# Performance work log

Hardware: AMD Instinct MI355X
Metric: run time of the kernel (lower is better)

The kernel has to match this reference:

```python
import jax, jax.numpy as jnp
import numpy as np

B = 256      # graph pairs
NPG = 28     # nodes per graph
MAXN = 32    # max_node_set_size
EPG = 64     # edges per graph (== max_edge_set_size, so no edge padding)
MAXE = 64
D = 128      # node_state_dim
FN = 32      # raw node feature dim
FE = 32      # raw edge feature dim
SK = 64      # sinkhorn_feature_dim
STEPS = 3    # propagation_steps
TEMP = 0.1
ITERS = 20
CW = 0.9     # consistency_weight
G = 2 * B
N = G * NPG
E = G * EPG


def _lin(key, fi, fo):
    return jax.random.normal(key, (fi, fo), jnp.float32) / np.sqrt(fi)


def setup_inputs() -> dict:
    key = jax.random.key(0)
    ks = jax.random.split(key, 12)
    rng = np.random.default_rng(0)
    off = (np.arange(G) * NPG)[:, None]   # graphs ordered q0,c0,q1,c1,...
    from_idx = jnp.asarray((rng.integers(0, NPG, (G, EPG)) + off).reshape(-1), jnp.int32)
    to_idx = jnp.asarray((rng.integers(0, NPG, (G, EPG)) + off).reshape(-1), jnp.int32)
    return dict(
        node_features=jax.random.normal(ks[0], (N, FN), jnp.float32),
        edge_features=jax.random.normal(ks[1], (E, FE), jnp.float32),
        enc_nw=_lin(ks[2], FN, D), enc_nb=jnp.zeros((D,), jnp.float32),
        enc_ew=_lin(ks[3], FE, D), enc_eb=jnp.zeros((D,), jnp.float32),
        msg_w1=_lin(ks[4], 3 * D, 2 * D), msg_b1=jnp.zeros((2 * D,), jnp.float32),
        msg_w2=_lin(ks[5], 2 * D, D), msg_b2=jnp.zeros((D,), jnp.float32),
        rmsg_w1=_lin(ks[6], 3 * D, 2 * D), rmsg_b1=jnp.zeros((2 * D,), jnp.float32),
        rmsg_w2=_lin(ks[7], 2 * D, D), rmsg_b2=jnp.zeros((D,), jnp.float32),
        upd_w1=_lin(ks[8], 2 * D, 2 * D), upd_b1=jnp.zeros((2 * D,), jnp.float32),
        upd_w2=_lin(ks[9], 2 * D, D), upd_b2=jnp.zeros((D,), jnp.float32),
        sk_w1=_lin(ks[10], D, SK), sk_b1=jnp.zeros((SK,), jnp.float32),
        sk_w2=_lin(ks[11], SK, SK), sk_b2=jnp.zeros((SK,), jnp.float32),
        from_idx=from_idx, to_idx=to_idx,
        query_sizes=jnp.full((B,), NPG, jnp.int32),
        corpus_sizes=jnp.full((B,), NPG, jnp.int32),
    )


def _mlp2(x, w1, b1, w2, b2):
    return jnp.maximum(x @ w1 + b1, 0.0) @ w2 + b2


def _sinkhorn(log_alpha):
    # log-domain sinkhorn (noise_factor = 0 -> deterministic)
    la = log_alpha / TEMP
    for _ in range(ITERS):
        la = la - jax.nn.logsumexp(la, axis=2, keepdims=True)
        la = la - jax.nn.logsumexp(la, axis=1, keepdims=True)
    return jnp.exp(la)


def _align(q, c, plan):
    # feature_alignment_score: -relu(q - P @ c).sum over set and feature dims
    return -jnp.maximum(q - plan @ c, 0.0).sum(axis=(1, 2))


def _forward(node_features, edge_features, enc_nw, enc_nb, enc_ew, enc_eb,
             msg_w1, msg_b1, msg_w2, msg_b2, rmsg_w1, rmsg_b1, rmsg_w2, rmsg_b2,
             upd_w1, upd_b1, upd_w2, upd_b2, sk_w1, sk_b1, sk_w2, sk_b2,
             from_idx, to_idx, query_sizes, corpus_sizes):
    h = node_features @ enc_nw + enc_nb        # encoder, [N, D]
    e = edge_features @ enc_ew + enc_eb        # [E, D]

    def messages(h):
        f = _mlp2(jnp.concatenate([h[from_idx], h[to_idx], e], -1), msg_w1, msg_b1, msg_w2, msg_b2)
        r = _mlp2(jnp.concatenate([h[to_idx], h[from_idx], e], -1), rmsg_w1, rmsg_b1, rmsg_w2, rmsg_b2)
        return f, r

    for _ in range(STEPS):  # GraphPropLayer x propagation_steps
        f, r = messages(h)
        agg = jax.ops.segment_sum(f, to_idx, num_segments=N) + \
              jax.ops.segment_sum(r, from_idx, num_segments=N)
        h = h + _mlp2(jnp.concatenate([agg, h], -1), upd_w1, upd_b1, upd_w2, upd_b2)

    # split_and_stack nodes: graphs alternate query/corpus, pad NPG -> MAXN
    hs = jnp.pad(h.reshape(B, 2, NPG, D), ((0, 0), (0, 0), (0, MAXN - NPG), (0, 0)))
    q_nodes, c_nodes = hs[:, 0], hs[:, 1]      # [B, MAXN, D]

    tq = _mlp2(q_nodes, sk_w1, sk_b1, sk_w2, sk_b2)
    tc = _mlp2(c_nodes, sk_w1, sk_b1, sk_w2, sk_b2)
    pos = jnp.arange(MAXN)[None, :]
    mq = tq * (pos < query_sizes[:, None])[..., None]
    mc = tc * (pos < corpus_sizes[:, None])[..., None]
    node_plan = _sinkhorn(jnp.einsum('bqd,bcd->bqc', mq, mc))   # [B, MAXN, MAXN]

    # propagation_messages on final node states
    f, r = messages(h)
    em = (f + r).reshape(B, 2, EPG, D)         # EPG == MAXE -> no pad
    q_edges, c_edges = em[:, 0], em[:, 1]

    # local (within-graph) endpoint indices for kronecker lookup
    fl = (from_idx % NPG).reshape(B, 2, EPG)
    tl = (to_idx % NPG).reshape(B, 2, EPG)
    qf, cf = fl[:, 0], fl[:, 1]
    qt, ct = tl[:, 0], tl[:, 1]

    def kron(T, qf, qt, cf, ct):
        straight = T[qf][:, cf] * T[qt][:, ct]   # [MAXE, MAXE]
        cross = T[qf][:, ct] * T[qt][:, cf]
        return straight + cross

    edge_scores = jax.vmap(kron)(node_plan, qf, qt, cf, ct)     # [B, MAXE, MAXE]
    edge_plan = _sinkhorn(edge_scores)

    return _align(q_nodes, c_nodes, node_plan) + CW * _align(q_edges, c_edges, edge_plan)


def reference(node_features, edge_features, enc_nw, enc_nb, enc_ew, enc_eb,
              msg_w1, msg_b1, msg_w2, msg_b2, rmsg_w1, rmsg_b1, rmsg_w2, rmsg_b2,
              upd_w1, upd_b1, upd_w2, upd_b2, sk_w1, sk_b1, sk_w2, sk_b2,
              from_idx, to_idx, query_sizes, corpus_sizes):
    return _forward(node_features, edge_features, enc_nw, enc_nb, enc_ew, enc_eb,
                    msg_w1, msg_b1, msg_w2, msg_b2, rmsg_w1, rmsg_b1, rmsg_w2, rmsg_b2,
                    upd_w1, upd_b1, upd_w2, upd_b2, sk_w1, sk_b1, sk_w2, sk_b2,
                    from_idx, to_idx, query_sizes, corpus_sizes)
```

## Files before the change

### kernel.cpp

```cpp
#include <hip/hip_runtime.h>
#include <math.h>

#define NPG 28
#define EPG 64
#define NB  256
#define NG  512
#define NN  14336
#define NE  32768
#define TEMPINV 10.0f
#define SINK_ITERS 20
#define CW 0.9f

typedef unsigned int uint;
typedef unsigned short ushort;
typedef __attribute__((ext_vector_type(8))) __bf16 bf16x8;
typedef __attribute__((ext_vector_type(4))) float f32x4;

__device__ __forceinline__ ushort f2bf(float x) {
    uint u = __float_as_uint(x);
    u += 0x7fffu + ((u >> 16) & 1u);
    return (ushort)(u >> 16);
}
__device__ __forceinline__ uint f2bf2(float lo, float hi) {
    return (uint)f2bf(lo) | ((uint)f2bf(hi) << 16);
}
__device__ __forceinline__ float bflo(uint w) { return __uint_as_float(w << 16); }
__device__ __forceinline__ float bfhi(uint w) { return __uint_as_float(w & 0xffff0000u); }
__device__ __forceinline__ uint relu_sum_pk(uint w1, uint w2, uint w3) {
    float lo = fmaxf(bflo(w1) + bflo(w2) + bflo(w3), 0.f);
    float hi = fmaxf(bfhi(w1) + bfhi(w2) + bfhi(w3), 0.f);
    return f2bf2(lo, hi);
}
__device__ __forceinline__ uint4 pack_f32x8(const float* src) {
    const float4 f0 = *(const float4*)src;
    const float4 f1 = *(const float4*)(src + 4);
    uint4 o;
    o.x = f2bf2(f0.x, f0.y);
    o.y = f2bf2(f0.z, f0.w);
    o.z = f2bf2(f1.x, f1.y);
    o.w = f2bf2(f1.z, f1.w);
    return o;
}
__device__ __forceinline__ f32x4 mfma16(bf16x8 a, bf16x8 b, f32x4 c) {
    return __builtin_amdgcn_mfma_f32_16x16x32_bf16(a, b, c, 0, 0, 0);
}

__global__ __launch_bounds__(512) void gnn_fused(
    const float* __restrict__ nf, const float* __restrict__ ef,
    const ushort* __restrict__ encL, const float* __restrict__ enc_nb,
    const ushort* __restrict__ WcombL, const float* __restrict__ bcomb,
    const ushort* __restrict__ WhpL,
    const ushort* __restrict__ W2fL, const ushort* __restrict__ W2rL,
    const float* __restrict__ b2f, const float* __restrict__ b2r,
    const ushort* __restrict__ UW1T, const float* __restrict__ ub1,
    const ushort* __restrict__ UW2T, const float* __restrict__ ub2,
    const int* __restrict__ from_idx, const int* __restrict__ to_idx,
    float* __restrict__ h, float* __restrict__ EM)
{
    __shared__ ushort HPs[NPG * 520];
    __shared__ ushort ECs[2 * 8 * 2048];
    __shared__ float acc_s[NPG * 132];
    __shared__ float hs[NPG * 132];
    __shared__ int fl[64], tl[64];
    const int g = blockIdx.x;
    const int tid = threadIdx.x;
    const int w = tid >> 6, lane = tid & 63;
    const int li = lane & 15, quad = lane >> 4;
    const int wm = w >> 1, wn = w & 1;
    ushort* hid = &HPs[0];

    if (tid < 64) {
        fl[tid] = from_idx[g * 64 + tid] - g * NPG;
        tl[tid] = to_idx[g * 64 + tid] - g * NPG;
    }

    {
        uint4 anf[2];
#pragma unroll
        for (int mi = 0; mi < 2; ++mi) {
            const int row = mi * 16 + li;
            const int rr = (row < NPG) ? row : 0;
            const float4 f0 = *(const float4*)(nf + ((size_t)g * NPG + rr) * 32 + quad * 8);
            const float4 f1 = *(const float4*)(nf + ((size_t)g * NPG + rr) * 32 + quad * 8 + 4);
            uint4 o;
            o.x = f2bf2(f0.x, f0.y); o.y = f2bf2(f0.z, f0.w);
            o.z = f2bf2(f1.x, f1.y); o.w = f2bf2(f1.z, f1.w);
            anf[mi] = o;
        }
        const int col = w * 16 + li;
        const bf16x8 b = __builtin_bit_cast(bf16x8,
            *(const uint4*)(encL + (size_t)col * 32 + quad * 8));
        f32x4 c0 = mfma16(__builtin_bit_cast(bf16x8, anf[0]), b, f32x4{0.f, 0.f, 0.f, 0.f});
        f32x4 c1 = mfma16(__builtin_bit_cast(bf16x8, anf[1]), b, f32x4{0.f, 0.f, 0.f, 0.f});
        const float bv = enc_nb[col];
#pragma unroll
        for (int r = 0; r < 4; ++r) {
            const int r0 = quad * 4 + r;
            hs[r0 * 132 + col] = c0[r] + bv;
            const int r1 = 16 + quad * 4 + r;
            if (r1 < NPG) hs[r1 * 132 + col] = c1[r] + bv;
        }
    }
    {
        uint4 aef[4];
#pragma unroll
        for (int mi = 0; mi < 4; ++mi) {
            const int e = mi * 16 + li;
            const float4 f0 = *(const float4*)(ef + ((size_t)g * 64 + e) * 32 + quad * 8);
            const float4 f1 = *(const float4*)(ef + ((size_t)g * 64 + e) * 32 + quad * 8 + 4);
            uint4 o;
            o.x = f2bf2(f0.x, f0.y); o.y = f2bf2(f0.z, f0.w);
            o.z = f2bf2(f1.x, f1.y); o.w = f2bf2(f1.z, f1.w);
            aef[mi] = o;
        }
#pragma unroll
        for (int ni = 0; ni < 4; ++ni) {
            const int col = w * 64 + ni * 16 + li;
            const bf16x8 b = __builtin_bit_cast(bf16x8,
                *(const uint4*)(WcombL + (size_t)col * 32 + quad * 8));
            const float bv = bcomb[col];
            const int pp = col >> 8, kbl = (col >> 5) & 7, j = col & 31;
#pragma unroll
            for (int mi = 0; mi < 4; ++mi) {
                f32x4 c = mfma16(__builtin_bit_cast(bf16x8, aef[mi]), b,
                                 f32x4{0.f, 0.f, 0.f, 0.f});
#pragma unroll
                for (int r = 0; r < 4; ++r) {
                    const int e = mi * 16 + quad * 4 + r;
                    ECs[pp * 16384 + kbl * 2048 + e * 32 + j] = f2bf(c[r] + bv);
                }
            }
        }
    }
    __syncthreads();

#pragma unroll 1
    for (int step = 0; step < 3; ++step) {
        uint4 ha[2][4];
#pragma unroll
        for (int mi = 0; mi < 2; ++mi) {
            const int row = mi * 16 + li;
            const int rr = (row < NPG) ? row : 0;
#pragma unroll
            for (int kb = 0; kb < 4; ++kb)
                ha[mi][kb] = pack_f32x8(&hs[rr * 132 + kb * 32 + quad * 8]);
        }
        for (int u = tid; u < NPG * 132; u += 512) acc_s[u] = 0.f;

        f32x4 acc[4];
#pragma unroll
        for (int j = 0; j < 4; ++j) acc[j] = f32x4{0.f, 0.f, 0.f, 0.f};

#pragma unroll 1
        for (int p = 0; p < 2; ++p) {
            {
                const int colw = w * 64;
#pragma unroll
                for (int ni = 0; ni < 4; ++ni) {
                    const int col = colw + ni * 16 + li;
                    const ushort* pb = WhpL + (size_t)(p * 512 + col) * 32 + quad * 8;
                    f32x4 c0 = f32x4{0.f, 0.f, 0.f, 0.f};
                    f32x4 c1 = f32x4{0.f, 0.f, 0.f, 0.f};
#pragma unroll
                    for (int kb = 0; kb < 4; ++kb) {
                        const bf16x8 b = __builtin_bit_cast(bf16x8,
                            *(const uint4*)(pb + (size_t)kb * 32768));
                        c0 = mfma16(__builtin_bit_cast(bf16x8, ha[0][kb]), b, c0);
                        c1 = mfma16(__builtin_bit_cast(bf16x8, ha[1][kb]), b, c1);
                    }
#pragma unroll
                    for (int r = 0; r < 4; ++r) {
                        const int r0 = quad * 4 + r;
                        HPs[r0 * 520 + col] = f2bf(c0[r]);
                        const int r1 = 16 + quad * 4 + r;
                        if (r1 < NPG) HPs[r1 * 520 + col] = f2bf(c1[r]);
                    }
                }
            }
            __syncthreads();

            if (p == 1) {
#pragma unroll
                for (int j = 0; j < 4; ++j) acc[j] = f32x4{0.f, 0.f, 0.f, 0.f};
            }
            const int e = wm * 16 + li;
            const int i1 = p ? tl[e] : fl[e];
            const int i2 = p ? fl[e] : tl[e];
            const int ad1 = i1 * 520 + quad * 8;
            const int ad2 = i2 * 520 + 256 + quad * 8;
            const int ade = p * 16384 + e * 32 + quad * 8;
            const ushort* W2L = p ? W2rL : W2fL;
            const int n0 = wn * 64;
            const ushort* pb[4];
#pragma unroll
            for (int ni = 0; ni < 4; ++ni)
                pb[ni] = W2L + (size_t)(n0 + ni * 16 + li) * 32 + quad * 8;
#pragma unroll
            for (int kb = 0; kb < 8; ++kb) {
                const uint4 u1 = *(const uint4*)&HPs[ad1 + kb * 32];
                const uint4 u2 = *(const uint4*)&HPs[ad2 + kb * 32];
                const uint4 ue = *(const uint4*)&ECs[ade + kb * 2048];
                uint4 o;
                o.x = relu_sum_pk(u1.x, u2.x, ue.x);
                o.y = relu_sum_pk(u1.y, u2.y, ue.y);
                o.z = relu_sum_pk(u1.z, u2.z, ue.z);
                o.w = relu_sum_pk(u1.w, u2.w, ue.w);
                const bf16x8 a = __builtin_bit_cast(bf16x8, o);
#pragma unroll
                for (int ni = 0; ni < 4; ++ni) {
                    const bf16x8 b = __builtin_bit_cast(bf16x8,
                        *(const uint4*)(pb[ni] + (size_t)kb * 4096));
                    acc[ni] = mfma16(a, b, acc[ni]);
                }
            }
            {
                const int* targ = p ? fl : tl;
                const float* bias = p ? b2r : b2f;
                float bv[4];
#pragma unroll
                for (int ni = 0; ni < 4; ++ni) bv[ni] = bias[n0 + ni * 16 + li];
#pragma unroll
                for (int r = 0; r < 4; ++r) {
                    const int loc = targ[wm * 16 + quad * 4 + r];
#pragma unroll
                    for (int ni = 0; ni < 4; ++ni)
                        atomicAdd(&acc_s[loc * 132 + n0 + ni * 16 + li],
                                  acc[ni][r] + bv[ni]);
                }
            }
            __syncthreads();
        }

        {
            const int n0u = w * 32;
            f32x4 ua[2][2];
#pragma unroll
            for (int mi = 0; mi < 2; ++mi)
#pragma unroll
                for (int ni = 0; ni < 2; ++ni) ua[mi][ni] = f32x4{0.f, 0.f, 0.f, 0.f};
            const ushort* pb0 = UW1T + (size_t)(n0u + li) * 256 + quad * 8;
            const ushort* pb1 = UW1T + (size_t)(n0u + 16 + li) * 256 + quad * 8;
#pragma unroll
            for (int kb = 0; kb < 8; ++kb) {
                bf16x8 a[2];
                if (kb < 4) {
#pragma unroll
                    for (int mi = 0; mi < 2; ++mi) {
                        const int row = mi * 16 + li;
                        const int rr = (row < NPG) ? row : 0;
                        a[mi] = __builtin_bit_cast(bf16x8,
                            pack_f32x8(&acc_s[rr * 132 + kb * 32 + quad * 8]));
                    }
                } else {
                    a[0] = __builtin_bit_cast(bf16x8, ha[0][kb - 4]);
                    a[1] = __builtin_bit_cast(bf16x8, ha[1][kb - 4]);
                }
                const bf16x8 b0 = __builtin_bit_cast(bf16x8, *(const uint4*)(pb0 + kb * 32));
                const bf16x8 b1 = __builtin_bit_cast(bf16x8, *(const uint4*)(pb1 + kb * 32));
#pragma unroll
                for (int mi = 0; mi < 2; ++mi) {
                    ua[mi][0] = mfma16(a[mi], b0, ua[mi][0]);
                    ua[mi][1] = mfma16(a[mi], b1, ua[mi][1]);
                }
            }
            const float bv0 = ub1[n0u + li], bv1 = ub1[n0u + 16 + li];
#pragma unroll
            for (int mi = 0; mi < 2; ++mi)
#pragma unroll
                for (int r = 0; r < 4; ++r) {
                    const int row = mi * 16 + quad * 4 + r;
                    if (row < NPG) {
                        hid[row * 264 + n0u + li] = f2bf(fmaxf(ua[mi][0][r] + bv0, 0.f));
                        hid[row * 264 + n0u + 16 + li] = f2bf(fmaxf(ua[mi][1][r] + bv1, 0.f));
                    }
                }
        }
        __syncthreads();
        {
            const int n0u = w * 16;
            f32x4 ua[2];
            ua[0] = f32x4{0.f, 0.f, 0.f, 0.f};
            ua[1] = f32x4{0.f, 0.f, 0.f, 0.f};
            const ushort* pb0 = UW2T + (size_t)(n0u + li) * 256 + quad * 8;
#pragma unroll
            for (int kb = 0; kb < 8; ++kb) {
                bf16x8 a[2];
#pragma unroll
                for (int mi = 0; mi < 2; ++mi) {
                    const int row = mi * 16 + li;
                    const int rr = (row < NPG) ? row : 0;
                    a[mi] = __builtin_bit_cast(bf16x8,
                        *(const uint4*)&hid[rr * 264 + kb * 32 + quad * 8]);
                }
                const bf16x8 b0 = __builtin_bit_cast(bf16x8, *(const uint4*)(pb0 + kb * 32));
                ua[0] = mfma16(a[0], b0, ua[0]);
                ua[1] = mfma16(a[1], b0, ua[1]);
            }
            const float bv = ub2[n0u + li];
#pragma unroll
            for (int mi = 0; mi < 2; ++mi)
#pragma unroll
                for (int r = 0; r < 4; ++r) {
                    const int row = mi * 16 + quad * 4 + r;
                    if (row < NPG)
                        hs[row * 132 + n0u + li] += ua[mi][r] + bv;
                }
        }
        __syncthreads();
    }

    {
        uint4 ha[2][4];
#pragma unroll
        for (int mi = 0; mi < 2; ++mi) {
            const int row = mi * 16 + li;
            const int rr = (row < NPG) ? row : 0;
#pragma unroll
            for (int kb = 0; kb < 4; ++kb)
                ha[mi][kb] = pack_f32x8(&hs[rr * 132 + kb * 32 + quad * 8]);
        }
        f32x4 acc[4];
#pragma unroll
        for (int j = 0; j < 4; ++j) acc[j] = f32x4{0.f, 0.f, 0.f, 0.f};
        const int n0 = wn * 64;
#pragma unroll 1
        for (int p = 0; p < 2; ++p) {
            {
                const int colw = w * 64;
#pragma unroll
                for (int ni = 0; ni < 4; ++ni) {
                    const int col = colw + ni * 16 + li;
                    const ushort* pb = WhpL + (size_t)(p * 512 + col) * 32 + quad * 8;
                    f32x4 c0 = f32x4{0.f, 0.f, 0.f, 0.f};
                    f32x4 c1 = f32x4{0.f, 0.f, 0.f, 0.f};
#pragma unroll
                    for (int kb = 0; kb < 4; ++kb) {
                        const bf16x8 b = __builtin_bit_cast(bf16x8,
                            *(const uint4*)(pb + (size_t)kb * 32768));
                        c0 = mfma16(__builtin_bit_cast(bf16x8, ha[0][kb]), b, c0);
                        c1 = mfma16(__builtin_bit_cast(bf16x8, ha[1][kb]), b, c1);
                    }
#pragma unroll
                    for (int r = 0; r < 4; ++r) {
                        const int r0 = quad * 4 + r;
                        HPs[r0 * 520 + col] = f2bf(c0[r]);
                        const int r1 = 16 + quad * 4 + r;
                        if (r1 < NPG) HPs[r1 * 520 + col] = f2bf(c1[r]);
                    }
                }
            }
            __syncthreads();
            const int e = wm * 16 + li;
            const int i1 = p ? tl[e] : fl[e];
            const int i2 = p ? fl[e] : tl[e];
            const int ad1 = i1 * 520 + quad * 8;
            const int ad2 = i2 * 520 + 256 + quad * 8;
            const int ade = p * 16384 + e * 32 + quad * 8;
            const ushort* W2L = p ? W2rL : W2fL;
            const ushort* pb[4];
#pragma unroll
            for (int ni = 0; ni < 4; ++ni)
                pb[ni] = W2L + (size_t)(n0 + ni * 16 + li) * 32 + quad * 8;
#pragma unroll
            for (int kb = 0; kb < 8; ++kb) {
                const uint4 u1 = *(const uint4*)&HPs[ad1 + kb * 32];
                const uint4 u2 = *(const uint4*)&HPs[ad2 + kb * 32];
                const uint4 ue = *(const uint4*)&ECs[ade + kb * 2048];
                uint4 o;
                o.x = relu_sum_pk(u1.x, u2.x, ue.x);
                o.y = relu_sum_pk(u1.y, u2.y, ue.y);
                o.z = relu_sum_pk(u1.z, u2.z, ue.z);
                o.w = relu_sum_pk(u1.w, u2.w, ue.w);
                const bf16x8 a = __builtin_bit_cast(bf16x8, o);
#pragma unroll
                for (int ni = 0; ni < 4; ++ni) {
                    const bf16x8 b = __builtin_bit_cast(bf16x8,
                        *(const uint4*)(pb[ni] + (size_t)kb * 4096));
                    acc[ni] = mfma16(a, b, acc[ni]);
                }
            }
            __syncthreads();
        }
        float bv[4];
#pragma unroll
        for (int ni = 0; ni < 4; ++ni)
            bv[ni] = b2f[n0 + ni * 16 + li] + b2r[n0 + ni * 16 + li];
#pragma unroll
        for (int r = 0; r < 4; ++r) {
            const int erow = g * 64 + wm * 16 + quad * 4 + r;
#pragma unroll
            for (int ni = 0; ni < 4; ++ni)
                EM[(size_t)erow * 128 + n0 + ni * 16 + li] = acc[ni][r] + bv[ni];
        }
    }
    for (int u = tid; u < NPG * 128; u += 512)
        h[(size_t)g * (NPG * 128) + u] = hs[(u >> 7) * 132 + (u & 127)];
}

__global__ __launch_bounds__(256) void pack2(
    const float* __restrict__ msg_w1, const float* __restrict__ rmsg_w1,
    const float* __restrict__ msg_b1, const float* __restrict__ rmsg_b1,
    const float* __restrict__ enc_ew, const float* __restrict__ enc_eb,
    const float* __restrict__ enc_nw,
    const float* __restrict__ msg_w2, const float* __restrict__ rmsg_w2,
    const float* __restrict__ upd_w1, const float* __restrict__ upd_w2,
    ushort* __restrict__ WcombL, float* __restrict__ bcomb,
    ushort* __restrict__ encL,
    ushort* __restrict__ WhpL, ushort* __restrict__ W2fL, ushort* __restrict__ W2rL,
    ushort* __restrict__ UW1T, ushort* __restrict__ UW2T)
{
    const int gid = blockIdx.x, tid = threadIdx.x;
    if (gid < 64) {
        const int idx = gid * 256 + tid;
        const int a = idx >> 9, n = idx & 511;
        const float* Wsrc = (n < 256) ? msg_w1 : rmsg_w1;
        const int nc = n & 255;
        float s = 0.f;
        for (int j = 0; j < 128; ++j)
            s = fmaf(enc_ew[a * 128 + j], Wsrc[(256 + j) * 256 + nc], s);
        WcombL[n * 32 + a] = f2bf(s);
    } else if (gid < 66) {
        const int n = (gid - 64) * 256 + tid;
        const float* Wsrc = (n < 256) ? msg_w1 : rmsg_w1;
        const float* bsrc = (n < 256) ? msg_b1 : rmsg_b1;
        const int nc = n & 255;
        float s = bsrc[nc];
        for (int j = 0; j < 128; ++j)
            s = fmaf(enc_eb[j], Wsrc[(256 + j) * 256 + nc], s);
        bcomb[n] = s;
    } else if (gid < 82) {
        const int idx = (gid - 66) * 256 + tid;
        const int n = idx >> 5, k = idx & 31;
        encL[idx] = f2bf(enc_nw[k * 128 + n]);
    } else if (gid < 594) {
        const int idx = (gid - 82) * 256 + tid;
        const int n = idx >> 7, k = idx & 127;
        const float* Wsrc = (n < 512) ? msg_w1 : rmsg_w1;
        const int part = (n >> 8) & 1, col = n & 255;
        WhpL[(size_t)(k >> 5) * 32768 + n * 32 + (k & 31)] =
            f2bf(Wsrc[(part * 128 + k) * 256 + col]);
    } else if (gid < 722) {
        const int idx = (gid - 594) * 256 + tid;
        const int n = idx >> 8, k = idx & 255;
        W2fL[(size_t)(k >> 5) * 4096 + n * 32 + (k & 31)] = f2bf(msg_w2[k * 128 + n]);
    } else if (gid < 850) {
        const int idx = (gid - 722) * 256 + tid;
        const int n = idx >> 8, k = idx & 255;
        W2rL[(size_t)(k >> 5) * 4096 + n * 32 + (k & 31)] = f2bf(rmsg_w2[k * 128 + n]);
    } else if (gid < 1106) {
        const int idx = (gid - 850) * 256 + tid;
        const int n = idx >> 8, k = idx & 255;
        UW1T[idx] = f2bf(upd_w1[k * 256 + n]);
    } else {
        const int idx = (gid - 1106) * 256 + tid;
        const int n = idx >> 8, k = idx & 255;
        UW2T[idx] = f2bf(upd_w2[k * 128 + n]);
    }
}

__global__ __launch_bounds__(256) void node_kernel(
    const float* __restrict__ h,
    const float* __restrict__ w1, const float* __restrict__ b1,
    const float* __restrict__ w2, const float* __restrict__ b2,
    const int* __restrict__ qsz, const int* __restrict__ csz,
    float* __restrict__ plan_out, float* __restrict__ loss_out)
{
    __shared__ float qn[32][128];
    __shared__ float cn[32][128];
    __shared__ float t1[32][64];
    __shared__ float mq[32][68];
    __shared__ float mc[32][68];
    __shared__ float la[32][33];
    __shared__ float red[4];
    const int bb = blockIdx.x;
    const int tid = threadIdx.x;
    const int qs = qsz[bb], cs = csz[bb];
    for (int u = tid * 4; u < 4096; u += 1024) {
        const int p = u >> 7, d = u & 127;
        float4 zq = make_float4(0.f, 0.f, 0.f, 0.f), zc = zq;
        if (p < NPG) {
            zq = *(const float4*)(h + (size_t)((2 * bb) * NPG + p) * 128 + d);
            zc = *(const float4*)(h + (size_t)((2 * bb + 1) * NPG + p) * 128 + d);
        }
        *(float4*)&qn[p][d] = zq;
        *(float4*)&cn[p][d] = zc;
    }
    __syncthreads();
    const int col = tid & 63;
    const int rg  = tid >> 6;
    for (int s = 0; s < 2; ++s) {
        const float (*src)[128] = s ? cn : qn;
        float (*dst)[68] = s ? mc : mq;
        const int sz = s ? cs : qs;
        float a8[8];
#pragma unroll
        for (int u = 0; u < 8; ++u) a8[u] = b1[col];
        for (int k = 0; k < 128; ++k) {
            const float wv = w1[k * 64 + col];
#pragma unroll
            for (int u = 0; u < 8; ++u) a8[u] = fmaf(src[rg + 4 * u][k], wv, a8[u]);
        }
#pragma unroll
        for (int u = 0; u < 8; ++u) t1[rg + 4 * u][col] = fmaxf(a8[u], 0.f);
        __syncthreads();
#pragma unroll
        for (int u = 0; u < 8; ++u) a8[u] = b2[col];
        for (int k = 0; k < 64; ++k) {
            const float wv = w2[k * 64 + col];
#pragma unroll
            for (int u = 0; u < 8; ++u) a8[u] = fmaf(t1[rg + 4 * u][k], wv, a8[u]);
        }
#pragma unroll
        for (int u = 0; u < 8; ++u) {
            const int r = rg + 4 * u;
            dst[r][col] = (r < sz) ? a8[u] : 0.f;
        }
        __syncthreads();
    }
    {
        const int q = tid >> 3, cg = tid & 7;
#pragma unroll
        for (int u = 0; u < 4; ++u) {
            const int c = cg + 8 * u;
            float s = 0.f;
            for (int d = 0; d < 64; ++d) s = fmaf(mq[q][d], mc[c][d], s);
            la[q][c] = s * TEMPINV;
        }
    }
    __syncthreads();
    const int l8 = tid & 7, rq = tid >> 3;
    for (int it = 0; it < SINK_ITERS; ++it) {
        {
            float x[4];
#pragma unroll
            for (int u = 0; u < 4; ++u) x[u] = la[rq][l8 * 4 + u];
            float m = fmaxf(fmaxf(x[0], x[1]), fmaxf(x[2], x[3]));
            m = fmaxf(m, __shfl_xor(m, 1));
            m = fmaxf(m, __shfl_xor(m, 2));
            m = fmaxf(m, __shfl_xor(m, 4));
            float s = __expf(x[0] - m) + __expf(x[1] - m) + __expf(x[2] - m) + __expf(x[3] - m);
            s += __shfl_xor(s, 1);
            s += __shfl_xor(s, 2);
            s += __shfl_xor(s, 4);
            const float lse = m + __logf(s);
#pragma unroll
            for (int u = 0; u < 4; ++u) la[rq][l8 * 4 + u] = x[u] - lse;
        }
        __syncthreads();
        {
            float x[4];
#pragma unroll
            for (int u = 0; u < 4; ++u) x[u] = la[l8 * 4 + u][rq];
            float m = fmaxf(fmaxf(x[0], x[1]), fmaxf(x[2], x[3]));
            m = fmaxf(m, __shfl_xor(m, 1));
            m = fmaxf(m, __shfl_xor(m, 2));
            m = fmaxf(m, __shfl_xor(m, 4));
            float s = __expf(x[0] - m) + __expf(x[1] - m) + __expf(x[2] - m) + __expf(x[3] - m);
            s += __shfl_xor(s, 1);
            s += __shfl_xor(s, 2);
            s += __shfl_xor(s, 4);
            const float lse = m + __logf(s);
#pragma unroll
            for (int u = 0; u < 4; ++u) la[l8 * 4 + u][rq] = x[u] - lse;
        }
        __syncthreads();
    }
    for (int u = tid; u < 1024; u += 256) {
        const int q = u >> 5, c = u & 31;
        const float p = __expf(la[q][c]);
        la[q][c] = p;
        plan_out[(size_t)bb * 1024 + u] = p;
    }
    __syncthreads();
    float lsum = 0.f;
    {
        const int q = tid >> 3, dg = tid & 7;
        for (int u = 0; u < 16; ++u) {
            const int d = dg + 8 * u;
            float pc = 0.f;
#pragma unroll
            for (int c = 0; c < 32; ++c) pc = fmaf(la[q][c], cn[c][d], pc);
            lsum += fmaxf(qn[q][d] - pc, 0.f);
        }
    }
#pragma unroll
    for (int off = 1; off < 64; off <<= 1) lsum += __shfl_xor(lsum, off);
    if ((tid & 63) == 0) red[tid >> 6] = lsum;
    __syncthreads();
    if (tid == 0) loss_out[bb] = -(red[0] + red[1] + red[2] + red[3]);
}

__global__ __launch_bounds__(256) void edge_kernel(
    const float* __restrict__ plan, const float* __restrict__ EM,
    const int* __restrict__ from_idx, const int* __restrict__ to_idx,
    float* __restrict__ loss_out)
{
    __shared__ float T[32][33];
    __shared__ float la[64][65];
    __shared__ float ce[64][128];
    __shared__ int qf[64], qt[64], cfi[64], cti[64];
    __shared__ float red[4];
    const int bb = blockIdx.x;
    const int tid = threadIdx.x;
    for (int u = tid; u < 1024; u += 256) T[u >> 5][u & 31] = plan[(size_t)bb * 1024 + u];
    if (tid < 64) {
        const int gq = 2 * bb, gc = 2 * bb + 1;
        qf[tid]  = from_idx[gq * 64 + tid] - gq * NPG;
        qt[tid]  = to_idx  [gq * 64 + tid] - gq * NPG;
        cfi[tid] = from_idx[gc * 64 + tid] - gc * NPG;
        cti[tid] = to_idx  [gc * 64 + tid] - gc * NPG;
    }
    {
        const int gc = 2 * bb + 1;
        for (int u = tid * 4; u < 8192; u += 1024) {
            const int i = u >> 7, d = u & 127;
            *(float4*)&ce[i][d] = *(const float4*)(EM + (size_t)(gc * 64 + i) * 128 + d);
        }
    }
    __syncthreads();
    {
        const int i = tid >> 2, jg = tid & 3;
        const int a = qf[i], b_ = qt[i];
#pragma unroll
        for (int u = 0; u < 16; ++u) {
            const int j = jg * 16 + u;
            const float s = T[a][cfi[j]] * T[b_][cti[j]] + T[a][cti[j]] * T[b_][cfi[j]];
            la[i][j] = s * TEMPINV;
        }
    }
    __syncthreads();
    const int l4 = tid & 3, rr = tid >> 2;
    for (int it = 0; it < SINK_ITERS; ++it) {
        {
            float x[16];
#pragma unroll
            for (int u = 0; u < 16; ++u) x[u] = la[rr][l4 * 16 + u];
            float m = x[0];
#pragma unroll
            for (int u = 1; u < 16; ++u) m = fmaxf(m, x[u]);
            m = fmaxf(m, __shfl_xor(m, 1));
            m = fmaxf(m, __shfl_xor(m, 2));
            float s = 0.f;
#pragma unroll
            for (int u = 0; u < 16; ++u) s += __expf(x[u] - m);
            s += __shfl_xor(s, 1);
            s += __shfl_xor(s, 2);
            const float lse = m + __logf(s);
#pragma unroll
            for (int u = 0; u < 16; ++u) la[rr][l4 * 16 + u] = x[u] - lse;
        }
        __syncthreads();
        {
            float x[16];
#pragma unroll
            for (int u = 0; u < 16; ++u) x[u] = la[l4 * 16 + u][rr];
            float m = x[0];
#pragma unroll
            for (int u = 1; u < 16; ++u) m = fmaxf(m, x[u]);
            m = fmaxf(m, __shfl_xor(m, 1));
            m = fmaxf(m, __shfl_xor(m, 2));
            float s = 0.f;
#pragma unroll
            for (int u = 0; u < 16; ++u) s += __expf(x[u] - m);
            s += __shfl_xor(s, 1);
            s += __shfl_xor(s, 2);
            const float lse = m + __logf(s);
#pragma unroll
            for (int u = 0; u < 16; ++u) la[l4 * 16 + u][rr] = x[u] - lse;
        }
        __syncthreads();
    }
    for (int u = tid; u < 4096; u += 256) la[u >> 6][u & 63] = __expf(la[u >> 6][u & 63]);
    __syncthreads();
    float lsum = 0.f;
    {
        const int q = tid >> 2, dg = tid & 3;
        const float* qe = EM + (size_t)((2 * bb) * 64 + q) * 128;
        for (int u = 0; u < 32; ++u) {
            const int d = dg + 4 * u;
            float pc = 0.f;
            for (int c = 0; c < 64; ++c) pc = fmaf(la[q][c], ce[c][d], pc);
            lsum += fmaxf(qe[d] - pc, 0.f);
        }
    }
#pragma unroll
    for (int off = 1; off < 64; off <<= 1) lsum += __shfl_xor(lsum, off);
    if ((tid & 63) == 0) red[tid >> 6] = lsum;
    __syncthreads();
    if (tid == 0) loss_out[bb] -= CW * (red[0] + red[1] + red[2] + red[3]);
}

extern "C" void kernel_launch(void* const* d_in, const int* in_sizes, int n_in,
                              void* d_out, int out_size, void* d_ws, size_t ws_size,
                              hipStream_t stream)
{
    const float* node_features = (const float*)d_in[0];
    const float* edge_features = (const float*)d_in[1];
    const float* enc_nw  = (const float*)d_in[2];
    const float* enc_nb  = (const float*)d_in[3];
    const float* enc_ew  = (const float*)d_in[4];
    const float* enc_eb  = (const float*)d_in[5];
    const float* msg_w1  = (const float*)d_in[6];
    const float* msg_b1  = (const float*)d_in[7];
    const float* msg_w2  = (const float*)d_in[8];
    const float* msg_b2  = (const float*)d_in[9];
    const float* rmsg_w1 = (const float*)d_in[10];
    const float* rmsg_b1 = (const float*)d_in[11];
    const float* rmsg_w2 = (const float*)d_in[12];
    const float* rmsg_b2 = (const float*)d_in[13];
    const float* upd_w1  = (const float*)d_in[14];
    const float* upd_b1  = (const float*)d_in[15];
    const float* upd_w2  = (const float*)d_in[16];
    const float* upd_b2  = (const float*)d_in[17];
    const float* sk_w1   = (const float*)d_in[18];
    const float* sk_b1   = (const float*)d_in[19];
    const float* sk_w2   = (const float*)d_in[20];
    const float* sk_b2   = (const float*)d_in[21];
    const int* from_idx  = (const int*)d_in[22];
    const int* to_idx    = (const int*)d_in[23];
    const int* qsizes    = (const int*)d_in[24];
    const int* csizes    = (const int*)d_in[25];
    float* out = (float*)d_out;

    float* ws     = (float*)d_ws;
    float* h      = ws;
    float* EM     = h + (size_t)NN * 128;
    float* plan   = EM + (size_t)NE * 128;
    float* bcomb  = plan + (size_t)NB * 1024;
    ushort* WcombL = (ushort*)(bcomb + 512);
    ushort* encL  = WcombL + 16384;
    ushort* WhpL  = encL + 4096;
    ushort* W2fL  = WhpL + 131072;
    ushort* W2rL  = W2fL + 32768;
    ushort* UW1T  = W2rL + 32768;
    ushort* UW2T  = UW1T + 65536;

    const dim3 blk(256);
    const dim3 blk512(512);

    pack2<<<1234, blk, 0, stream>>>(msg_w1, rmsg_w1, msg_b1, rmsg_b1,
                                    enc_ew, enc_eb, enc_nw, msg_w2, rmsg_w2,
                                    upd_w1, upd_w2,
                                    WcombL, bcomb, encL, WhpL, W2fL, W2rL, UW1T, UW2T);

    gnn_fused<<<dim3(NG), blk512, 0, stream>>>(
        node_features, edge_features, encL, enc_nb, WcombL, bcomb,
        WhpL, W2fL, W2rL, msg_b2, rmsg_b2,
        UW1T, upd_b1, UW2T, upd_b2, from_idx, to_idx, h, EM);

    node_kernel<<<NB, blk, 0, stream>>>(
        h, sk_w1, sk_b1, sk_w2, sk_b2, qsizes, csizes, plan, out);
    edge_kernel<<<NB, blk, 0, stream>>>(
        plan, EM, from_idx, to_idx, out);
}
```

Measured before the change: 468.9 us.

## Compute both message-direction projections in one pass and fuse node/edge head kernels

In the GNN propagation kernel, the per-direction HP projection (two passes, each followed by a barrier) is replaced by a single pass in which each wave computes 128 columns into a widened shared buffer. This removes two barriers per step and one barrier inside the forward/reverse loops. The node-sinkhorn and edge-sinkhorn kernels are merged into one, so the node plan stays in shared memory instead of round-tripping through global memory, and one launch is dropped. The cost is more LDS per block (a larger HPs buffer plus the merged head's shared arrays), which may lower occupancy.

Result: slower. 594.8 us (+26.8%).

```diff
diff --git a/kernel.cpp b/kernel.cpp
--- a/kernel.cpp
+++ b/kernel.cpp
@@ -44,6 +44,8 @@
 __device__ __forceinline__ f32x4 mfma16(bf16x8 a, bf16x8 b, f32x4 c) {
     return __builtin_amdgcn_mfma_f32_16x16x32_bf16(a, b, c, 0, 0, 0);
 }
+
+#define HPSTR 1032
 
 __global__ __launch_bounds__(512) void gnn_fused(
     const float* __restrict__ nf, const float* __restrict__ ef,
@@ -57,7 +59,7 @@
     const int* __restrict__ from_idx, const int* __restrict__ to_idx,
     float* __restrict__ h, float* __restrict__ EM)
 {
-    __shared__ ushort HPs[NPG * 520];
+    __shared__ ushort HPs[NPG * HPSTR];
     __shared__ ushort ECs[2 * 8 * 2048];
     __shared__ float acc_s[NPG * 132];
     __shared__ float hs[NPG * 132];
@@ -147,47 +149,39 @@
         }
         for (int u = tid; u < NPG * 132; u += 512) acc_s[u] = 0.f;
 
-        f32x4 acc[4];
-#pragma unroll
-        for (int j = 0; j < 4; ++j) acc[j] = f32x4{0.f, 0.f, 0.f, 0.f};
+        {
+            const int cw = w * 128;
+#pragma unroll
+            for (int ni = 0; ni < 8; ++ni) {
+                const int c = cw + ni * 16 + li;
+                const ushort* pb = WhpL + (size_t)c * 32 + quad * 8;
+                f32x4 c0 = f32x4{0.f, 0.f, 0.f, 0.f};
+                f32x4 c1 = f32x4{0.f, 0.f, 0.f, 0.f};
+#pragma unroll
+                for (int kb = 0; kb < 4; ++kb) {
+                    const bf16x8 b = __builtin_bit_cast(bf16x8,
+                        *(const uint4*)(pb + (size_t)kb * 32768));
+                    c0 = mfma16(__builtin_bit_cast(bf16x8, ha[0][kb]), b, c0);
+                    c1 = mfma16(__builtin_bit_cast(bf16x8, ha[1][kb]), b, c1);
+                }
+#pragma unroll
+                for (int r = 0; r < 4; ++r) {
+                    const int r0 = quad * 4 + r;
+                    HPs[r0 * HPSTR + c] = f2bf(c0[r]);
+                    const int r1 = 16 + quad * 4 + r;
+                    if (r1 < NPG) HPs[r1 * HPSTR + c] = f2bf(c1[r]);
+                }
+            }
+        }
+        __syncthreads();
 
 #pragma unroll 1
         for (int p = 0; p < 2; ++p) {
-            {
-                const int colw = w * 64;
-#pragma unroll
-                for (int ni = 0; ni < 4; ++ni) {
-                    const int col = colw + ni * 16 + li;
-                    const ushort* pb = WhpL + (size_t)(p * 512 + col) * 32 + quad * 8;
-                    f32x4 c0 = f32x4{0.f, 0.f, 0.f, 0.f};
-                    f32x4 c1 = f32x4{0.f, 0.f, 0.f, 0.f};
-#pragma unroll
-                    for (int kb = 0; kb < 4; ++kb) {
-                        const bf16x8 b = __builtin_bit_cast(bf16x8,
-                            *(const uint4*)(pb + (size_t)kb * 32768));
-                        c0 = mfma16(__builtin_bit_cast(bf16x8, ha[0][kb]), b, c0);
-                        c1 = mfma16(__builtin_bit_cast(bf16x8, ha[1][kb]), b, c1);
-                    }
-#pragma unroll
-                    for (int r = 0; r < 4; ++r) {
-                        const int r0 = quad * 4 + r;
-                        HPs[r0 * 520 + col] = f2bf(c0[r]);
-                        const int r1 = 16 + quad * 4 + r;
-                        if (r1 < NPG) HPs[r1 * 520 + col] = f2bf(c1[r]);
-                    }
-                }
-            }
-            __syncthreads();
-
-            if (p == 1) {
-#pragma unroll
-                for (int j = 0; j < 4; ++j) acc[j] = f32x4{0.f, 0.f, 0.f, 0.f};
-            }
             const int e = wm * 16 + li;
             const int i1 = p ? tl[e] : fl[e];
             const int i2 = p ? fl[e] : tl[e];
-            const int ad1 = i1 * 520 + quad * 8;
-            const int ad2 = i2 * 520 + 256 + quad * 8;
+            const int ad1 = i1 * HPSTR + p * 512 + quad * 8;
+            const int ad2 = i2 * HPSTR + p * 512 + 256 + quad * 8;
             const int ade = p * 16384 + e * 32 + quad * 8;
             const ushort* W2L = p ? W2rL : W2fL;
             const int n0 = wn * 64;
@@ -195,6 +189,9 @@
 #pragma unroll
             for (int ni = 0; ni < 4; ++ni)
                 pb[ni] = W2L + (size_t)(n0 + ni * 16 + li) * 32 + quad * 8;
+            f32x4 acc[4];
+#pragma unroll
+            for (int j = 0; j < 4; ++j) acc[j] = f32x4{0.f, 0.f, 0.f, 0.f};
 #pragma unroll
             for (int kb = 0; kb < 8; ++kb) {
                 const uint4 u1 = *(const uint4*)&HPs[ad1 + kb * 32];
@@ -228,8 +225,8 @@
                                   acc[ni][r] + bv[ni]);
                 }
             }
-            __syncthreads();
-        }
+        }
+        __syncthreads();
 
         {
             const int n0u = w * 32;
@@ -319,42 +316,42 @@
             for (int kb = 0; kb < 4; ++kb)
                 ha[mi][kb] = pack_f32x8(&hs[rr * 132 + kb * 32 + quad * 8]);
         }
+        {
+            const int cw = w * 128;
+#pragma unroll
+            for (int ni = 0; ni < 8; ++ni) {
+                const int c = cw + ni * 16 + li;
+                const ushort* pb = WhpL + (size_t)c * 32 + quad * 8;
+                f32x4 c0 = f32x4{0.f, 0.f, 0.f, 0.f};
+                f32x4 c1 = f32x4{0.f, 0.f, 0.f, 0.f};
+#pragma unroll
+                for (int kb = 0; kb < 4; ++kb) {
+                    const bf16x8 b = __builtin_bit_cast(bf16x8,
+                        *(const uint4*)(pb + (size_t)kb * 32768));
+                    c0 = mfma16(__builtin_bit_cast(bf16x8, ha[0][kb]), b, c0);
+                    c1 = mfma16(__builtin_bit_cast(bf16x8, ha[1][kb]), b, c1);
+                }
+#pragma unroll
+                for (int r = 0; r < 4; ++r) {
+                    const int r0 = quad * 4 + r;
+                    HPs[r0 * HPSTR + c] = f2bf(c0[r]);
+                    const int r1 = 16 + quad * 4 + r;
+                    if (r1 < NPG) HPs[r1 * HPSTR + c] = f2bf(c1[r]);
+                }
+            }
+        }
+        __syncthreads();
         f32x4 acc[4];
 #pragma unroll
         for (int j = 0; j < 4; ++j) acc[j] = f32x4{0.f, 0.f, 0.f, 0.f};
         const int n0 = wn * 64;
 #pragma unroll 1
         for (int p = 0; p < 2; ++p) {
-            {
-                const int colw = w * 64;
-#pragma unroll
-                for (int ni = 0; ni < 4; ++ni) {
-                    const int col = colw + ni * 16 + li;
-                    const ushort* pb = WhpL + (size_t)(p * 512 + col) * 32 + quad * 8;
-                    f32x4 c0 = f32x4{0.f, 0.f, 0.f, 0.f};
-                    f32x4 c1 = f32x4{0.f, 0.f, 0.f, 0.f};
-#pragma unroll
-                    for (int kb = 0; kb < 4; ++kb) {
-                        const bf16x8 b = __builtin_bit_cast(bf16x8,
-                            *(const uint4*)(pb + (size_t)kb * 32768));
-                        c0 = mfma16(__builtin_bit_cast(bf16x8, ha[0][kb]), b, c0);
-                        c1 = mfma16(__builtin_bit_cast(bf16x8, ha[1][kb]), b, c1);
-                    }
-#pragma unroll
-                    for (int r = 0; r < 4; ++r) {
-                        const int r0 = quad * 4 + r;
-                        HPs[r0 * 520 + col] = f2bf(c0[r]);
-                        const int r1 = 16 + quad * 4 + r;
-                        if (r1 < NPG) HPs[r1 * 520 + col] = f2bf(c1[r]);
-                    }
-                }
-            }
-            __syncthreads();
             const int e = wm * 16 + li;
             const int i1 = p ? tl[e] : fl[e];
             const int i2 = p ? fl[e] : tl[e];
-            const int ad1 = i1 * 520 + quad * 8;
-            const int ad2 = i2 * 520 + 256 + quad * 8;
+            const int ad1 = i1 * HPSTR + p * 512 + quad * 8;
+            const int ad2 = i2 * HPSTR + p * 512 + 256 + quad * 8;
             const int ade = p * 16384 + e * 32 + quad * 8;
             const ushort* W2L = p ? W2rL : W2fL;
             const ushort* pb[4];
@@ -379,7 +376,6 @@
                     acc[ni] = mfma16(a, b, acc[ni]);
                 }
             }
-            __syncthreads();
         }
         float bv[4];
 #pragma unroll
@@ -458,23 +454,29 @@
     }
 }
 
-__global__ __launch_bounds__(256) void node_kernel(
-    const float* __restrict__ h,
+__global__ __launch_bounds__(256) void heads_fused(
+    const float* __restrict__ h, const float* __restrict__ EM,
     const float* __restrict__ w1, const float* __restrict__ b1,
     const float* __restrict__ w2, const float* __restrict__ b2,
     const int* __restrict__ qsz, const int* __restrict__ csz,
-    float* __restrict__ plan_out, float* __restrict__ loss_out)
+    const int* __restrict__ from_idx, const int* __restrict__ to_idx,
+    float* __restrict__ loss_out)
 {
     __shared__ float qn[32][128];
     __shared__ float cn[32][128];
     __shared__ float t1[32][64];
     __shared__ float mq[32][68];
     __shared__ float mc[32][68];
-    __shared__ float la[32][33];
+    __shared__ float la32[32][33];
+    __shared__ float la64[64][65];
+    __shared__ float ce[64][128];
+    __shared__ int qf[64], qt[64], cfi[64], cti[64];
     __shared__ float red[4];
+    __shared__ float nodeloss;
     const int bb = blockIdx.x;
     const int tid = threadIdx.x;
     const int qs = qsz[bb], cs = csz[bb];
+
     for (int u = tid * 4; u < 4096; u += 1024) {
         const int p = u >> 7, d = u & 127;
         float4 zq = make_float4(0.f, 0.f, 0.f, 0.f), zc = zq;
@@ -485,7 +487,22 @@
         *(float4*)&qn[p][d] = zq;
         *(float4*)&cn[p][d] = zc;
     }
+    if (tid < 64) {
+        const int gq = 2 * bb, gc = 2 * bb + 1;
+        qf[tid]  = from_idx[gq * 64 + tid] - gq * NPG;
+        qt[tid]  = to_idx  [gq * 64 + tid] - gq * NPG;
+        cfi[tid] = from_idx[gc * 64 + tid] - gc * NPG;
+        cti[tid] = to_idx  [gc * 64 + tid] - gc * NPG;
+    }
+    {
+        const int gc = 2 * bb + 1;
+        for (int u = tid * 4; u < 8192; u += 1024) {
+            const int i = u >> 7, d = u & 127;
+            *(float4*)&ce[i][d] = *(const float4*)(EM + (size_t)(gc * 64 + i) * 128 + d);
+        }
+    }
     __syncthreads();
+
     const int col = tid & 63;
     const int rg  = tid >> 6;
     for (int s = 0; s < 2; ++s) {
@@ -524,170 +541,146 @@
             const int c = cg + 8 * u;
             float s = 0.f;
             for (int d = 0; d < 64; ++d) s = fmaf(mq[q][d], mc[c][d], s);
-            la[q][c] = s * TEMPINV;
+            la32[q][c] = s * TEMPINV;
         }
     }
     __syncthreads();
-    const int l8 = tid & 7, rq = tid >> 3;
-    for (int it = 0; it < SINK_ITERS; ++it) {
-        {
-            float x[4];
-#pragma unroll
-            for (int u = 0; u < 4; ++u) x[u] = la[rq][l8 * 4 + u];
-            float m = fmaxf(fmaxf(x[0], x[1]), fmaxf(x[2], x[3]));
-            m = fmaxf(m, __shfl_xor(m, 1));
-            m = fmaxf(m, __shfl_xor(m, 2));
-            m = fmaxf(m, __shfl_xor(m, 4));
-            float s = __expf(x[0] - m) + __expf(x[1] - m) + __expf(x[2] - m) + __expf(x[3] - m);
-            s += __shfl_xor(s, 1);
-            s += __shfl_xor(s, 2);
-            s += __shfl_xor(s, 4);
-            const float lse = m + __logf(s);
-#pragma unroll
-            for (int u = 0; u < 4; ++u) la[rq][l8 * 4 + u] = x[u] - lse;
-        }
-        __syncthreads();
-        {
-            float x[4];
-#pragma unroll
-            for (int u = 0; u < 4; ++u) x[u] = la[l8 * 4 + u][rq];
-            float m = fmaxf(fmaxf(x[0], x[1]), fmaxf(x[2], x[3]));
-            m = fmaxf(m, __shfl_xor(m, 1));
-            m = fmaxf(m, __shfl_xor(m, 2));
-            m = fmaxf(m, __shfl_xor(m, 4));
-            float s = __expf(x[0] - m) + __expf(x[1] - m) + __expf(x[2] - m) + __expf(x[3] - m);
-            s += __shfl_xor(s, 1);
-            s += __shfl_xor(s, 2);
-            s += __shfl_xor(s, 4);
-            const float lse = m + __logf(s);
-#pragma unroll
-            for (int u = 0; u < 4; ++u) la[l8 * 4 + u][rq] = x[u] - lse;
-        }
-        __syncthreads();
+    {
+        const int l8 = tid & 7, rq = tid >> 3;
+        for (int it = 0; it < SINK_ITERS; ++it) {
+            {
+                float x[4];
+#pragma unroll
+                for (int u = 0; u < 4; ++u) x[u] = la32[rq][l8 * 4 + u];
+                float m = fmaxf(fmaxf(x[0], x[1]), fmaxf(x[2], x[3]));
+                m = fmaxf(m, __shfl_xor(m, 1));
+                m = fmaxf(m, __shfl_xor(m, 2));
+                m = fmaxf(m, __shfl_xor(m, 4));
+                float s = __expf(x[0] - m) + __expf(x[1] - m) + __expf(x[2] - m) + __expf(x[3] - m);
+                s += __shfl_xor(s, 1);
+                s += __shfl_xor(s, 2);
+                s += __shfl_xor(s, 4);
+                const float lse = m + __logf(s);
+#pragma unroll
+                for (int u = 0; u < 4; ++u) la32[rq][l8 * 4 + u] = x[u] - lse;
+            }
+            __syncthreads();
+            {
+                float x[4];
+#pragma unroll
+                for (int u = 0; u < 4; ++u) x[u] = la32[l8 * 4 + u][rq];
+                float m = fmaxf(fmaxf(x[0], x[1]), fmaxf(x[2], x[3]));
+                m = fmaxf(m, __shfl_xor(m, 1));
+                m = fmaxf(m, __shfl_xor(m, 2));
+                m = fmaxf(m, __shfl_xor(m, 4));
+                float s = __expf(x[0] - m) + __expf(x[1] - m) + __expf(x[2] - m) + __expf(x[3] - m);
+                s += __shfl_xor(s, 1);
+                s += __shfl_xor(s, 2);
+                s += __shfl_xor(s, 4);
+                const float lse = m + __logf(s);
+#pragma unroll
+                for (int u = 0; u < 4; ++u) la32[l8 * 4 + u][rq] = x[u] - lse;
+            }
+            __syncthreads();
+        }
     }
     for (int u = tid; u < 1024; u += 256) {
         const int q = u >> 5, c = u & 31;
-        const float p = __expf(la[q][c]);
-        la[q][c] = p;
-        plan_out[(size_t)bb * 1024 + u] = p;
+        la32[q][c] = __expf(la32[q][c]);
     }
     __syncthreads();
-    float lsum = 0.f;
-    {
+    {
+        float lsum = 0.f;
         const int q = tid >> 3, dg = tid & 7;
         for (int u = 0; u < 16; ++u) {
             const int d = dg + 8 * u;
             float pc = 0.f;
 #pragma unroll
-            for (int c = 0; c < 32; ++c) pc = fmaf(la[q][c], cn[c][d], pc);
+            for (int c = 0; c < 32; ++c) pc = fmaf(la32[q][c], cn[c][d], pc);
             lsum += fmaxf(qn[q][d] - pc, 0.f);
         }
-    }
-#pragma unroll
-    for (int off = 1; off < 64; off <<= 1) lsum += __shfl_xor(lsum, off);
-    if ((tid & 63) == 0) red[tid >> 6] = lsum;
+#pragma unroll
+        for (int off = 1; off < 64; off <<= 1) lsum += __shfl_xor(lsum, off);
+        if ((tid & 63) == 0) red[tid >> 6] = lsum;
+        __syncthreads();
+        if (tid == 0) nodeloss = red[0] + red[1] + red[2] + red[3];
+    }
     __syncthreads();
-    if (tid == 0) loss_out[bb] = -(red[0] + red[1] + red[2] + red[3]);
-}
-
-__global__ __launch_bounds__(256) void edge_kernel(
-    const float* __restrict__ plan, const float* __restrict__ EM,
-    const int* __restrict__ from_idx, const int* __restrict__ to_idx,
-    float* __restrict__ loss_out)
-{
-    __shared__ float T[32][33];
-    __shared__ float la[64][65];
-    __shared__ float ce[64][128];
-    __shared__ int qf[64], qt[64], cfi[64], cti[64];
-    __shared__ float red[4];
-    const int bb = blockIdx.x;
-    const int tid = threadIdx.x;
-    for (int u = tid; u < 1024; u += 256) T[u >> 5][u & 31] = plan[(size_t)bb * 1024 + u];
-    if (tid < 64) {
-        const int gq = 2 * bb, gc = 2 * bb + 1;
-        qf[tid]  = from_idx[gq * 64 + tid] - gq * NPG;
-        qt[tid]  = to_idx  [gq * 64 + tid] - gq * NPG;
-        cfi[tid] = from_idx[gc * 64 + tid] - gc * NPG;
-        cti[tid] = to_idx  [gc * 64 + tid] - gc * NPG;
-    }
-    {
-        const int gc = 2 * bb + 1;
-        for (int u = tid * 4; u < 8192; u += 1024) {
-            const int i = u >> 7, d = u & 127;
-            *(float4*)&ce[i][d] = *(const float4*)(EM + (size_t)(gc * 64 + i) * 128 + d);
-        }
-    }
-    __syncthreads();
+
     {
         const int i = tid >> 2, jg = tid & 3;
         const int a = qf[i], b_ = qt[i];
 #pragma unroll
         for (int u = 0; u < 16; ++u) {
             const int j = jg * 16 + u;
-            const float s = T[a][cfi[j]] * T[b_][cti[j]] + T[a][cti[j]] * T[b_][cfi[j]];
-            la[i][j] = s * TEMPINV;
+            const float s = la32[a][cfi[j]] * la32[b_][cti[j]] +
+                            la32[a][cti[j]] * la32[b_][cfi[j]];
+            la64[i][j] = s * TEMPINV;
         }
     }
     __syncthreads();
-    const int l4 = tid & 3, rr = tid >> 2;
-    for (int it = 0; it < SINK_ITERS; ++it) {
-        {
-            float x[16];
-#pragma unroll
-            for (int u = 0; u < 16; ++u) x[u] = la[rr][l4 * 16 + u];
-            float m = x[0];
-#pragma unroll
-            for (int u = 1; u < 16; ++u) m = fmaxf(m, x[u]);
-            m = fmaxf(m, __shfl_xor(m, 1));
-            m = fmaxf(m, __shfl_xor(m, 2));
-            float s = 0.f;
-#pragma unroll
-            for (int u = 0; u < 16; ++u) s += __expf(x[u] - m);
-            s += __shfl_xor(s, 1);
-            s += __shfl_xor(s, 2);
-            const float lse = m + __logf(s);
-#pragma unroll
-            for (int u = 0; u < 16; ++u) la[rr][l4 * 16 + u] = x[u] - lse;
-        }
-        __syncthreads();
-        {
-            float x[16];
-#pragma unroll
-            for (int u = 0; u < 16; ++u) x[u] = la[l4 * 16 + u][rr];
-            float m = x[0];
-#pragma unroll
-            for (int u = 1; u < 16; ++u) m = fmaxf(m, x[u]);
-            m = fmaxf(m, __shfl_xor(m, 1));
-            m = fmaxf(m, __shfl_xor(m, 2));
-            float s = 0.f;
-#pragma unroll
-            for (int u = 0; u < 16; ++u) s += __expf(x[u] - m);
-            s += __shfl_xor(s, 1);
-            s += __shfl_xor(s, 2);
-            const float lse = m + __logf(s);
-#pragma unroll
-            for (int u = 0; u < 16; ++u) la[l4 * 16 + u][rr] = x[u] - lse;
-        }
-        __syncthreads();
-    }
-    for (int u = tid; u < 4096; u += 256) la[u >> 6][u & 63] = __expf(la[u >> 6][u & 63]);
+    {
+        const int l4 = tid & 3, rr = tid >> 2;
+        for (int it = 0; it < SINK_ITERS; ++it) {
+            {
+                float x[16];
+#pragma unroll
+                for (int u = 0; u < 16; ++u) x[u] = la64[rr][l4 * 16 + u];
+                float m = x[0];
+#pragma unroll
+                for (int u = 1; u < 16; ++u) m = fmaxf(m, x[u]);
+                m = fmaxf(m, __shfl_xor(m, 1));
+                m = fmaxf(m, __shfl_xor(m, 2));
+                float s = 0.f;
+#pragma unroll
+                for (int u = 0; u < 16; ++u) s += __expf(x[u] - m);
+                s += __shfl_xor(s, 1);
+                s += __shfl_xor(s, 2);
+                const float lse = m + __logf(s);
+#pragma unroll
+                for (int u = 0; u < 16; ++u) la64[rr][l4 * 16 + u] = x[u] - lse;
+            }
+            __syncthreads();
+            {
+                float x[16];
+#pragma unroll
+                for (int u = 0; u < 16; ++u) x[u] = la64[l4 * 16 + u][rr];
+                float m = x[0];
+#pragma unroll
+                for (int u = 1; u < 16; ++u) m = fmaxf(m, x[u]);
+                m = fmaxf(m, __shfl_xor(m, 1));
+                m = fmaxf(m, __shfl_xor(m, 2));
+                float s = 0.f;
+#pragma unroll
+                for (int u = 0; u < 16; ++u) s += __expf(x[u] - m);
+                s += __shfl_xor(s, 1);
+                s += __shfl_xor(s, 2);
+                const float lse = m + __logf(s);
+#pragma unroll
+                for (int u = 0; u < 16; ++u) la64[l4 * 16 + u][rr] = x[u] - lse;
+            }
+            __syncthreads();
+        }
+    }
+    for (int u = tid; u < 4096; u += 256) la64[u >> 6][u & 63] = __expf(la64[u >> 6][u & 63]);
     __syncthreads();
-    float lsum = 0.f;
-    {
+    {
+        float lsum = 0.f;
         const int q = tid >> 2, dg = tid & 3;
         const float* qe = EM + (size_t)((2 * bb) * 64 + q) * 128;
         for (int u = 0; u < 32; ++u) {
             const int d = dg + 4 * u;
             float pc = 0.f;
-            for (int c = 0; c < 64; ++c) pc = fmaf(la[q][c], ce[c][d], pc);
+            for (int c = 0; c < 64; ++c) pc = fmaf(la64[q][c], ce[c][d], pc);
             lsum += fmaxf(qe[d] - pc, 0.f);
         }
-    }
-#pragma unroll
-    for (int off = 1; off < 64; off <<= 1) lsum += __shfl_xor(lsum, off);
-    if ((tid & 63) == 0) red[tid >> 6] = lsum;
-    __syncthreads();
-    if (tid == 0) loss_out[bb] -= CW * (red[0] + red[1] + red[2] + red[3]);
+#pragma unroll
+        for (int off = 1; off < 64; off <<= 1) lsum += __shfl_xor(lsum, off);
+        if ((tid & 63) == 0) red[tid >> 6] = lsum;
+        __syncthreads();
+        if (tid == 0)
+            loss_out[bb] = -nodeloss - CW * (red[0] + red[1] + red[2] + red[3]);
+    }
 }
 
 extern "C" void kernel_launch(void* const* d_in, const int* in_sizes, int n_in,
@@ -725,8 +718,7 @@
     float* ws     = (float*)d_ws;
     float* h      = ws;
     float* EM     = h + (size_t)NN * 128;
-    float* plan   = EM + (size_t)NE * 128;
-    float* bcomb  = plan + (size_t)NB * 1024;
+    float* bcomb  = EM + (size_t)NE * 128;
     ushort* WcombL = (ushort*)(bcomb + 512);
     ushort* encL  = WcombL + 16384;
     ushort* WhpL  = encL + 4096;
@@ -748,8 +740,7 @@
         WhpL, W2fL, W2rL, msg_b2, rmsg_b2,
         UW1T, upd_b1, UW2T, upd_b2, from_idx, to_idx, h, EM);
 
-    node_kernel<<<NB, blk, 0, stream>>>(
-        h, sk_w1, sk_b1, sk_w2, sk_b2, qsizes, csizes, plan, out);
-    edge_kernel<<<NB, blk, 0, stream>>>(
-        plan, EM, from_idx, to_idx, out);
-}
+    heads_fused<<<NB, blk, 0, stream>>>(
+        h, EM, sk_w1, sk_b1, sk_w2, sk_b2, qsizes, csizes,
+        from_idx, to_idx, out);
+}
```
